# Kernel optimization log

Measured on AMD Instinct MI355X. Metric: run time of the kernel, lower is better.

Reference implementation:

```python
import jax, jax.numpy as jnp
import numpy as np
from jax import lax

BS, L, HID = 16, 512, 768
H, HD, NREG = 12, 64, 8
R2 = 2 * NREG


def setup_inputs() -> dict:
    key = jax.random.key(0)
    ks = jax.random.split(key, 7)
    s = 1.0 / np.sqrt(HID)
    return {
        "hidden_states": jax.random.normal(ks[0], (BS, L, HID), jnp.float32),
        "K1_w": jax.random.normal(ks[1], (H * HD, HID), jnp.float32) * s,
        "K1_b": jnp.zeros((H * HD,), jnp.float32),
        "V1_w": jax.random.normal(ks[2], (H * HD, HID), jnp.float32) * s,
        "V1_b": jnp.zeros((H * HD,), jnp.float32),
        "reading_head": jax.random.normal(ks[3], (H, HD), jnp.float32) * (1.0 / np.sqrt(HD)),
        "bidirection_weight": jnp.ones((1, 1, H, 1, R2), jnp.float32) * (1.0 / R2),
    }


def _softmax_dim1(x):
    # torch: softmax over length dim (1) plus 1/exp(max) residual term
    m = jnp.max(x, axis=1, keepdims=True)
    e = jnp.exp(x - m)
    return e / jnp.sum(e, axis=1, keepdims=True) + jnp.exp(-m)


def _cummax_idx(e):
    # torch.cummax indices over axis=1 for a bool tensor (ties -> latest index):
    # last True index so far; if no True yet, current index.
    ar = jnp.arange(e.shape[1], dtype=jnp.int32)[None, :, None]
    lt = lax.cummax(jnp.where(e, ar, jnp.int32(-1)), axis=1)
    return jnp.where(lt >= 0, lt, ar)


def reference(hidden_states, K1_w, K1_b, V1_w, V1_b, reading_head, bidirection_weight):
    bs, length, _ = hidden_states.shape
    K1 = jax.nn.relu(hidden_states @ K1_w.T + K1_b).reshape(bs, length, H, HD)
    V1 = jax.nn.relu(hidden_states @ V1_w.T + V1_b).reshape(bs, length, H, HD)

    scores = jnp.einsum("blhn,hn->blh", K1, reading_head)
    events = _softmax_dim1(scores) > (1.5 / length)  # (bs, L, H) bool; fwd==bwd for IC1

    col0 = _cummax_idx(events)  # (bs, L, H)
    rolled = jnp.roll(events, -1, axis=1)
    col1 = jnp.flip(512 - _cummax_idx(jnp.flip(rolled, axis=1)), axis=1)
    col1 = col1.at[:, 0].set(0)

    # sequential shift-register scan over length
    e_seq = jnp.moveaxis(events, 1, 0)  # (L, bs, H)
    f_seq = jnp.moveaxis(col0, 1, 0)
    b_seq = jnp.moveaxis(col1, 1, 0)
    row0 = jnp.concatenate(
        [f_seq[0][:, None], b_seq[0][:, None], jnp.zeros((bs, R2, H), jnp.int32)], axis=1
    )  # (bs, R2+2, H)

    def step(row, inp):
        e, f, b = inp
        reg = jnp.where(e[:, None, :], row[:, :-2], row[:, 2:])  # shift-in on event
        new_row = jnp.concatenate([f[:, None], b[:, None], reg], axis=1)
        return new_row, reg

    _, regs = lax.scan(step, row0, (e_seq[1:], f_seq[1:], b_seq[1:]))
    regs = jnp.concatenate([jnp.zeros((1, bs, R2, H), jnp.int32), regs], axis=0)  # (L,bs,R2,H)
    idx = jnp.moveaxis(regs, 0, 1).reshape(bs, length * R2, H)
    idx = jnp.clip(idx, 0, length - 1)

    V2 = jnp.take_along_axis(V1, idx[..., None], axis=1).reshape(bs, length, R2, H, HD)
    w = bidirection_weight.reshape(H, R2)
    return jnp.einsum("blrhd,hr->blhd", V2, w)  # (bs, L, H, HD)
```

## Files before the change

kernel.cpp:

```cpp
#include <hip/hip_runtime.h>
#include <cstdint>
#include <cstddef>

#define BSZ 16
#define LQ  512
#define HIDDIM 768
#define NH  12
#define HD  64
#define R2V 16
#define NTOT 1536
#define MTOT 8192

typedef __bf16 bf16x8 __attribute__((ext_vector_type(8)));
typedef float  f32x4  __attribute__((ext_vector_type(4)));

__device__ inline unsigned short f2bf(float x) {
    union { float f; unsigned u; } c; c.f = x;
    unsigned r = c.u + 0x7fffu + ((c.u >> 16) & 1u);
    return (unsigned short)(r >> 16);
}
__device__ inline float bfl(unsigned u) { return __uint_as_float(u << 16); }
__device__ inline float bfh(unsigned u) { return __uint_as_float(u & 0xffff0000u); }

#define NHS4 1572864
#define NW1  147456
#define NW4  294912

__global__ __launch_bounds__(256) void cast_pack(
    const float* __restrict__ hs,
    const float* __restrict__ Kw, const float* __restrict__ Vw,
    const float* __restrict__ Kb, const float* __restrict__ Vb,
    unsigned short* __restrict__ hsb, unsigned short* __restrict__ Wb,
    float* __restrict__ biasp)
{
    const int i = blockIdx.x * 256 + threadIdx.x;
    float4 v; unsigned short* dst;
    if (i < NHS4) {
        v = ((const float4*)hs)[i];
        dst = hsb + (size_t)i * 4;
    } else {
        const int j = i - NHS4;
        v = (j < NW1) ? ((const float4*)Kw)[j] : ((const float4*)Vw)[j - NW1];
        dst = Wb + (size_t)j * 4;
    }
    ushort4 o;
    o.x = f2bf(v.x); o.y = f2bf(v.y); o.z = f2bf(v.z); o.w = f2bf(v.w);
    *(ushort4*)dst = o;
    if (i < 768) { biasp[i] = Kb[i]; biasp[768 + i] = Vb[i]; }
}

#define TBM 128
#define TBN 128
#define TBK 32
#define KITERS (HIDDIM / TBK)

#define GLD16(g, l) __builtin_amdgcn_global_load_lds( \
    (const __attribute__((address_space(1))) void*)(g), \
    (__attribute__((address_space(3))) void*)(l), 16, 0, 0)

__global__ __launch_bounds__(256) void gemm_mfma(
    const unsigned short* __restrict__ Abf,
    const unsigned short* __restrict__ Wbf,
    const float* __restrict__ biasp,
    unsigned short* __restrict__ K1b, unsigned short* __restrict__ V1b)
{
    __shared__ unsigned short As[2][TBM * TBK];
    __shared__ unsigned short Bs[2][TBN * TBK];

    const int n0   = blockIdx.x * TBN;
    const int m0   = blockIdx.y * TBM;
    const int tid  = threadIdx.x;
    const int wid  = tid >> 6;
    const int lane = tid & 63;
    const int wm   = (wid & 1) * 64;
    const int wn   = (wid >> 1) * 64;

    f32x4 acc[4][4] = {};

    const int r0 = wid * 32;
    const int rA = r0 + (lane >> 2);
    const int kp = (lane & 3) * 8;

    const unsigned short* Ap0 = Abf + (size_t)(m0 + rA) * HIDDIM + kp;
    const unsigned short* Ap1 = Abf + (size_t)(m0 + rA + 16) * HIDDIM + kp;
    const unsigned short* Bp0 = Wbf + (size_t)(n0 + rA) * HIDDIM + kp;
    const unsigned short* Bp1 = Wbf + (size_t)(n0 + rA + 16) * HIDDIM + kp;

    const int fm = lane & 15;
    const int fk = (lane >> 4) * 8;

#define STAGE(buf, kof)                                        \
    do {                                                       \
        GLD16(Ap0 + (kof), &As[buf][r0 * TBK]);                \
        GLD16(Ap1 + (kof), &As[buf][(r0 + 16) * TBK]);         \
        GLD16(Bp0 + (kof), &Bs[buf][r0 * TBK]);                \
        GLD16(Bp1 + (kof), &Bs[buf][(r0 + 16) * TBK]);         \
    } while (0)

    STAGE(0, 0);

    for (int it = 0; it < KITERS; ++it) {
        __syncthreads();
        if (it + 1 < KITERS) STAGE((it + 1) & 1, (it + 1) * TBK);
        const int cb = it & 1;

        bf16x8 af[4], bfr[4];
        #pragma unroll
        for (int mi = 0; mi < 4; ++mi)
            af[mi] = *reinterpret_cast<const bf16x8*>(&As[cb][(wm + mi * 16 + fm) * TBK + fk]);
        #pragma unroll
        for (int ni = 0; ni < 4; ++ni)
            bfr[ni] = *reinterpret_cast<const bf16x8*>(&Bs[cb][(wn + ni * 16 + fm) * TBK + fk]);
        #pragma unroll
        for (int mi = 0; mi < 4; ++mi)
            #pragma unroll
            for (int ni = 0; ni < 4; ++ni)
                acc[mi][ni] = __builtin_amdgcn_mfma_f32_16x16x32_bf16(
                    bfr[ni], af[mi], acc[mi][ni], 0, 0, 0);
    }
#undef STAGE

    const bool isK = (n0 < HIDDIM);
    unsigned short* __restrict__ dst = isK ? K1b : V1b;
    const int nsub = isK ? 0 : HIDDIM;
    const int mloc = lane & 15;
    const int nq   = (lane >> 4) * 4;

    #pragma unroll
    for (int mi = 0; mi < 4; ++mi) {
        const int mg = m0 + wm + mi * 16 + mloc;
        #pragma unroll
        for (int ni = 0; ni < 4; ++ni) {
            const int ng = n0 + wn + ni * 16 + nq;
            float4 bv = *(const float4*)(biasp + ng);
            f32x4 a = acc[mi][ni];
            ushort4 o;
            o.x = f2bf(fmaxf(a[0] + bv.x, 0.f));
            o.y = f2bf(fmaxf(a[1] + bv.y, 0.f));
            o.z = f2bf(fmaxf(a[2] + bv.z, 0.f));
            o.w = f2bf(fmaxf(a[3] + bv.w, 0.f));
            *(ushort4*)(dst + (size_t)mg * HIDDIM + (ng - nsub)) = o;
        }
    }
}

#define SINF (1 << 30)
#define IXP 17

__global__ __launch_bounds__(512) void scan_gather(
    const unsigned short* __restrict__ K1b,
    const unsigned short* __restrict__ V1b,
    const float* __restrict__ rh,
    const float* __restrict__ bw,
    float* __restrict__ out)
{
    const int bh   = blockIdx.x;
    const int b    = bh / NH;
    const int h    = bh % NH;
    const int l    = threadIdx.x;
    const int lane = l & 63;
    const int wid  = l >> 6;

    __shared__ float wredA[8];
    __shared__ float wredB[8];
    __shared__ int   wp0[8];
    __shared__ int   wp1[8];
    __shared__ int   wp2[8];
    __shared__ int   ev[LQ];
    __shared__ int   col0[LQ];
    __shared__ int   col1[LQ];
    __shared__ int   E[LQ];
    __shared__ int   idxs[LQ * IXP];
    __shared__ float wsm[R2V];

    if (l < R2V) wsm[l] = bw[h * R2V + l];

    const unsigned short* krow = K1b + ((size_t)(b * LQ + l)) * HIDDIM + h * HD;
    const float* rrow = rh + h * HD;
    float s = 0.f;
    #pragma unroll
    for (int c8 = 0; c8 < 8; ++c8) {
        uint4 kv = *(const uint4*)(krow + c8 * 8);
        float4 ra = *(const float4*)(rrow + c8 * 8);
        float4 rb = *(const float4*)(rrow + c8 * 8 + 4);
        s += bfl(kv.x) * ra.x + bfh(kv.x) * ra.y
           + bfl(kv.y) * ra.z + bfh(kv.y) * ra.w
           + bfl(kv.z) * rb.x + bfh(kv.z) * rb.y
           + bfl(kv.w) * rb.z + bfh(kv.w) * rb.w;
    }

    float mx = s;
    #pragma unroll
    for (int off = 32; off > 0; off >>= 1) mx = fmaxf(mx, __shfl_xor(mx, off));
    if (lane == 0) wredA[wid] = mx;
    __syncthreads();
    float m = wredA[0];
    #pragma unroll
    for (int i = 1; i < 8; ++i) m = fmaxf(m, wredA[i]);

    const float e = expf(s - m);
    float sm = e;
    #pragma unroll
    for (int off = 32; off > 0; off >>= 1) sm += __shfl_xor(sm, off);
    if (lane == 0) wredB[wid] = sm;
    __syncthreads();
    float ssum = 0.f;
    #pragma unroll
    for (int i = 0; i < 8; ++i) ssum += wredB[i];

    const float p = e / ssum + expf(-m);
    const int event = (p > (1.5f / 512.0f)) ? 1 : 0;
    ev[l] = event;

    int v = event ? l : -1;
    #pragma unroll
    for (int off = 1; off < 64; off <<= 1) {
        int u = __shfl_up(v, off);
        if (lane >= off) v = (u > v) ? u : v;
    }
    if (lane == 63) wp0[wid] = v;
    __syncthreads();
    int pfx = -1;
    for (int i = 0; i < wid; ++i) pfx = (wp0[i] > pfx) ? wp0[i] : pfx;
    v = (pfx > v) ? pfx : v;
    col0[l] = (v >= 0) ? v : l;

    int v1 = ev[(l + 1) & (LQ - 1)] ? l : SINF;
    #pragma unroll
    for (int off = 1; off < 64; off <<= 1) {
        int u = __shfl_down(v1, off);
        if (lane < 64 - off) v1 = (u < v1) ? u : v1;
    }
    if (lane == 0) wp1[wid] = v1;
    __syncthreads();
    int sfx = SINF;
    for (int i = wid + 1; i < 8; ++i) sfx = (wp1[i] < sfx) ? wp1[i] : sfx;
    v1 = (sfx < v1) ? sfx : v1;
    col1[l] = (l == 0) ? 0 : (((v1 < SINF) ? v1 : l) + 1);

    int c = (l >= 1) ? event : 0;
    #pragma unroll
    for (int off = 1; off < 64; off <<= 1) {
        int u = __shfl_up(c, off);
        if (lane >= off) c += u;
    }
    if (lane == 63) wp2[wid] = c;
    __syncthreads();
    for (int i = 0; i < wid; ++i) c += wp2[i];

    if (l >= 1 && event) E[c - 1] = l;
    __syncthreads();

    int* op = &idxs[l * IXP];
    #pragma unroll
    for (int j = 0; j < 8; ++j) {
        const int k = c - 1 - j;
        int f = 0, bb = 0;
        if (k >= 0) {
            const int t = E[k];
            f  = col0[t - 1];
            bb = col1[t - 1];
        }
        op[2 * j]     = min(max(f, 0), LQ - 1);
        op[2 * j + 1] = min(max(bb, 0), LQ - 1);
    }
    __syncthreads();

    const int dsl = lane & 7;
    const size_t vbase = (size_t)b * LQ * HIDDIM + h * HD + dsl * 8;

    for (int round = 0; round < 8; ++round) {
        const int lg = round * 64 + wid * 8 + (lane >> 3);
        const int* ip = &idxs[lg * IXP];
        float a0 = 0.f, a1 = 0.f, a2 = 0.f, a3 = 0.f;
        float a4 = 0.f, a5 = 0.f, a6 = 0.f, a7 = 0.f;
        #pragma unroll 1
        for (int rc = 0; rc < R2V; rc += 4) {
            const int i0 = ip[rc], i1 = ip[rc + 1], i2 = ip[rc + 2], i3 = ip[rc + 3];
            uint4 v0 = *(const uint4*)(V1b + vbase + (size_t)i0 * HIDDIM);
            uint4 vA = *(const uint4*)(V1b + vbase + (size_t)i1 * HIDDIM);
            uint4 vB = *(const uint4*)(V1b + vbase + (size_t)i2 * HIDDIM);
            uint4 vC = *(const uint4*)(V1b + vbase + (size_t)i3 * HIDDIM);
            const float w0 = wsm[rc], w1 = wsm[rc + 1], w2 = wsm[rc + 2], w3 = wsm[rc + 3];
            a0 += w0 * bfl(v0.x); a1 += w0 * bfh(v0.x);
            a2 += w0 * bfl(v0.y); a3 += w0 * bfh(v0.y);
            a4 += w0 * bfl(v0.z); a5 += w0 * bfh(v0.z);
            a6 += w0 * bfl(v0.w); a7 += w0 * bfh(v0.w);
            a0 += w1 * bfl(vA.x); a1 += w1 * bfh(vA.x);
            a2 += w1 * bfl(vA.y); a3 += w1 * bfh(vA.y);
            a4 += w1 * bfl(vA.z); a5 += w1 * bfh(vA.z);
            a6 += w1 * bfl(vA.w); a7 += w1 * bfh(vA.w);
            a0 += w2 * bfl(vB.x); a1 += w2 * bfh(vB.x);
            a2 += w2 * bfl(vB.y); a3 += w2 * bfh(vB.y);
            a4 += w2 * bfl(vB.z); a5 += w2 * bfh(vB.z);
            a6 += w2 * bfl(vB.w); a7 += w2 * bfh(vB.w);
            a0 += w3 * bfl(vC.x); a1 += w3 * bfh(vC.x);
            a2 += w3 * bfl(vC.y); a3 += w3 * bfh(vC.y);
            a4 += w3 * bfl(vC.z); a5 += w3 * bfh(vC.z);
            a6 += w3 * bfl(vC.w); a7 += w3 * bfh(vC.w);
        }
        float* po = out + ((size_t)(b * LQ + lg) * NH + h) * HD + dsl * 8;
        *(float4*)po       = make_float4(a0, a1, a2, a3);
        *((float4*)po + 1) = make_float4(a4, a5, a6, a7);
    }
}

extern "C" void kernel_launch(void* const* d_in, const int* in_sizes, int n_in,
                              void* d_out, int out_size, void* d_ws, size_t ws_size,
                              hipStream_t stream)
{
    (void)in_sizes; (void)n_in; (void)out_size; (void)ws_size;

    const float* hs = (const float*)d_in[0];
    const float* Kw = (const float*)d_in[1];
    const float* Kb = (const float*)d_in[2];
    const float* Vw = (const float*)d_in[3];
    const float* Vb = (const float*)d_in[4];
    const float* rh = (const float*)d_in[5];
    const float* bw = (const float*)d_in[6];
    float* out = (float*)d_out;

    char* ws = (char*)d_ws;
    unsigned short* K1b   = (unsigned short*)(ws);
    unsigned short* V1b   = (unsigned short*)(ws + 12582912);
    unsigned short* hsb   = (unsigned short*)(ws + 25165824);
    unsigned short* Wb    = (unsigned short*)(ws + 37748736);
    float*          biasp = (float*)(ws + 40108032);

    cast_pack<<<(NHS4 + NW4) / 256, 256, 0, stream>>>(hs, Kw, Vw, Kb, Vb, hsb, Wb, biasp);

    dim3 g1(NTOT / TBN, MTOT / TBM);
    gemm_mfma<<<g1, 256, 0, stream>>>(hsb, Wb, biasp, K1b, V1b);

    scan_gather<<<BSZ * NH, LQ, 0, stream>>>(K1b, V1b, rh, bw, out);
}
```

Baseline: 145.7 us.

## Fuse fp32-to-bf16 cast into GEMM tile loads, drop separate cast kernel

Removes the standalone cast_pack kernel. The GEMM now reads fp32 activations and weights directly into registers, converts them to bf16 with packed conversions, and writes them into the double-buffered LDS tiles. Global loads for the next tile are issued before the MFMA work so they overlap with compute. This saves one kernel launch and the write and re-read of bf16 copies in exchiange for reading fp32 (twice the bytes per tile) from global memory on every GEMM block. It also gives up the asynchronous global_load_lds path and adds register pressure under the new occupancy hint of 3.

```diff
diff --git a/kernel.cpp b/kernel.cpp
--- a/kernel.cpp
+++ b/kernel.cpp
@@ -22,31 +22,15 @@
 __device__ inline float bfl(unsigned u) { return __uint_as_float(u << 16); }
 __device__ inline float bfh(unsigned u) { return __uint_as_float(u & 0xffff0000u); }
 
-#define NHS4 1572864
-#define NW1  147456
-#define NW4  294912
-
-__global__ __launch_bounds__(256) void cast_pack(
-    const float* __restrict__ hs,
-    const float* __restrict__ Kw, const float* __restrict__ Vw,
-    const float* __restrict__ Kb, const float* __restrict__ Vb,
-    unsigned short* __restrict__ hsb, unsigned short* __restrict__ Wb,
-    float* __restrict__ biasp)
-{
-    const int i = blockIdx.x * 256 + threadIdx.x;
-    float4 v; unsigned short* dst;
-    if (i < NHS4) {
-        v = ((const float4*)hs)[i];
-        dst = hsb + (size_t)i * 4;
-    } else {
-        const int j = i - NHS4;
-        v = (j < NW1) ? ((const float4*)Kw)[j] : ((const float4*)Vw)[j - NW1];
-        dst = Wb + (size_t)j * 4;
-    }
-    ushort4 o;
-    o.x = f2bf(v.x); o.y = f2bf(v.y); o.z = f2bf(v.z); o.w = f2bf(v.w);
-    *(ushort4*)dst = o;
-    if (i < 768) { biasp[i] = Kb[i]; biasp[768 + i] = Vb[i]; }
+__device__ inline unsigned pk2bf(float x, float y) {
+#if __has_builtin(__builtin_amdgcn_cvt_pk_bf16_f32)
+    typedef __bf16 bf16x2 __attribute__((ext_vector_type(2)));
+    union { bf16x2 v; unsigned u; } c;
+    c.v = __builtin_amdgcn_cvt_pk_bf16_f32(x, y);
+    return c.u;
+#else
+    return (unsigned)f2bf(x) | ((unsigned)f2bf(y) << 16);
+#endif
 }
 
 #define TBM 128
@@ -54,14 +38,10 @@
 #define TBK 32
 #define KITERS (HIDDIM / TBK)
 
-#define GLD16(g, l) __builtin_amdgcn_global_load_lds( \
-    (const __attribute__((address_space(1))) void*)(g), \
-    (__attribute__((address_space(3))) void*)(l), 16, 0, 0)
-
-__global__ __launch_bounds__(256) void gemm_mfma(
-    const unsigned short* __restrict__ Abf,
-    const unsigned short* __restrict__ Wbf,
-    const float* __restrict__ biasp,
+__global__ __launch_bounds__(256, 3) void gemm_fused(
+    const float* __restrict__ hs,
+    const float* __restrict__ Kw, const float* __restrict__ Vw,
+    const float* __restrict__ Kb, const float* __restrict__ Vb,
     unsigned short* __restrict__ K1b, unsigned short* __restrict__ V1b)
 {
     __shared__ unsigned short As[2][TBM * TBK];
@@ -75,34 +55,65 @@
     const int wm   = (wid & 1) * 64;
     const int wn   = (wid >> 1) * 64;
 
+    const bool isK = (n0 < HIDDIM);
+    const float* __restrict__ Wsrc = isK ? Kw : Vw;
+    const float* __restrict__ bias = isK ? Kb : Vb;
+    const int ncol0 = isK ? n0 : (n0 - HIDDIM);
+
     f32x4 acc[4][4] = {};
 
     const int r0 = wid * 32;
-    const int rA = r0 + (lane >> 2);
-    const int kp = (lane & 3) * 8;
-
-    const unsigned short* Ap0 = Abf + (size_t)(m0 + rA) * HIDDIM + kp;
-    const unsigned short* Ap1 = Abf + (size_t)(m0 + rA + 16) * HIDDIM + kp;
-    const unsigned short* Bp0 = Wbf + (size_t)(n0 + rA) * HIDDIM + kp;
-    const unsigned short* Bp1 = Wbf + (size_t)(n0 + rA + 16) * HIDDIM + kp;
+    const int rA = r0 + (lane >> 1);
+    const int kh = (lane & 1) * 16;
+
+    const float* Aptr = hs   + (size_t)(m0 + rA) * HIDDIM + kh;
+    const float* Bptr = Wsrc + (size_t)(ncol0 + rA) * HIDDIM + kh;
+
+    uint4* AsD = (uint4*)&As[0][rA * TBK + kh];
+    uint4* BsD = (uint4*)&Bs[0][rA * TBK + kh];
+    const int bufStride16 = (TBM * TBK) / 8;
+
+    float4 ar0, ar1, ar2, ar3, br0, br1, br2, br3;
+
+#define LOADREGS(kof)                                     \
+    do {                                                  \
+        ar0 = *(const float4*)(Aptr + (kof));             \
+        ar1 = *(const float4*)(Aptr + (kof) + 4);         \
+        ar2 = *(const float4*)(Aptr + (kof) + 8);         \
+        ar3 = *(const float4*)(Aptr + (kof) + 12);        \
+        br0 = *(const float4*)(Bptr + (kof));             \
+        br1 = *(const float4*)(Bptr + (kof) + 4);         \
+        br2 = *(const float4*)(Bptr + (kof) + 8);         \
+        br3 = *(const float4*)(Bptr + (kof) + 12);        \
+    } while (0)
+
+#define CVTSTORE(buf)                                                         \
+    do {                                                                      \
+        uint4 p;                                                              \
+        p.x = pk2bf(ar0.x, ar0.y); p.y = pk2bf(ar0.z, ar0.w);                 \
+        p.z = pk2bf(ar1.x, ar1.y); p.w = pk2bf(ar1.z, ar1.w);                 \
+        AsD[(buf) * bufStride16] = p;                                         \
+        p.x = pk2bf(ar2.x, ar2.y); p.y = pk2bf(ar2.z, ar2.w);                 \
+        p.z = pk2bf(ar3.x, ar3.y); p.w = pk2bf(ar3.z, ar3.w);                 \
+        AsD[(buf) * bufStride16 + 1] = p;                                     \
+        p.x = pk2bf(br0.x, br0.y); p.y = pk2bf(br0.z, br0.w);                 \
+        p.z = pk2bf(br1.x, br1.y); p.w = pk2bf(br1.z, br1.w);                 \
+        BsD[(buf) * bufStride16] = p;                                         \
+        p.x = pk2bf(br2.x, br2.y); p.y = pk2bf(br2.z, br2.w);                 \
+        p.z = pk2bf(br3.x, br3.y); p.w = pk2bf(br3.z, br3.w);                 \
+        BsD[(buf) * bufStride16 + 1] = p;                                     \
+    } while (0)
 
     const int fm = lane & 15;
     const int fk = (lane >> 4) * 8;
 
-#define STAGE(buf, kof)                                        \
-    do {                                                       \
-        GLD16(Ap0 + (kof), &As[buf][r0 * TBK]);                \
-        GLD16(Ap1 + (kof), &As[buf][(r0 + 16) * TBK]);         \
-        GLD16(Bp0 + (kof), &Bs[buf][r0 * TBK]);                \
-        GLD16(Bp1 + (kof), &Bs[buf][(r0 + 16) * TBK]);         \
-    } while (0)
-
-    STAGE(0, 0);
+    LOADREGS(0);
+    CVTSTORE(0);
 
     for (int it = 0; it < KITERS; ++it) {
         __syncthreads();
-        if (it + 1 < KITERS) STAGE((it + 1) & 1, (it + 1) * TBK);
         const int cb = it & 1;
+        if (it + 1 < KITERS) LOADREGS((it + 1) * TBK);
 
         bf16x8 af[4], bfr[4];
         #pragma unroll
@@ -117,12 +128,13 @@
             for (int ni = 0; ni < 4; ++ni)
                 acc[mi][ni] = __builtin_amdgcn_mfma_f32_16x16x32_bf16(
                     bfr[ni], af[mi], acc[mi][ni], 0, 0, 0);
-    }
-#undef STAGE
-
-    const bool isK = (n0 < HIDDIM);
+
+        if (it + 1 < KITERS) CVTSTORE(cb ^ 1);
+    }
+#undef LOADREGS
+#undef CVTSTORE
+
     unsigned short* __restrict__ dst = isK ? K1b : V1b;
-    const int nsub = isK ? 0 : HIDDIM;
     const int mloc = lane & 15;
     const int nq   = (lane >> 4) * 4;
 
@@ -131,15 +143,15 @@
         const int mg = m0 + wm + mi * 16 + mloc;
         #pragma unroll
         for (int ni = 0; ni < 4; ++ni) {
-            const int ng = n0 + wn + ni * 16 + nq;
-            float4 bv = *(const float4*)(biasp + ng);
+            const int col = ncol0 + wn + ni * 16 + nq;
+            float4 bv = *(const float4*)(bias + col);
             f32x4 a = acc[mi][ni];
             ushort4 o;
             o.x = f2bf(fmaxf(a[0] + bv.x, 0.f));
             o.y = f2bf(fmaxf(a[1] + bv.y, 0.f));
             o.z = f2bf(fmaxf(a[2] + bv.z, 0.f));
             o.w = f2bf(fmaxf(a[3] + bv.w, 0.f));
-            *(ushort4*)(dst + (size_t)mg * HIDDIM + (ng - nsub)) = o;
+            *(ushort4*)(dst + (size_t)mg * HIDDIM + col) = o;
         }
     }
 }
@@ -321,16 +333,11 @@
     float* out = (float*)d_out;
 
     char* ws = (char*)d_ws;
-    unsigned short* K1b   = (unsigned short*)(ws);
-    unsigned short* V1b   = (unsigned short*)(ws + 12582912);
-    unsigned short* hsb   = (unsigned short*)(ws + 25165824);
-    unsigned short* Wb    = (unsigned short*)(ws + 37748736);
-    float*          biasp = (float*)(ws + 40108032);
-
-    cast_pack<<<(NHS4 + NW4) / 256, 256, 0, stream>>>(hs, Kw, Vw, Kb, Vb, hsb, Wb, biasp);
+    unsigned short* K1b = (unsigned short*)(ws);
+    unsigned short* V1b = (unsigned short*)(ws + 12582912);
 
     dim3 g1(NTOT / TBN, MTOT / TBM);
-    gemm_mfma<<<g1, 256, 0, stream>>>(hsb, Wb, biasp, K1b, V1b);
+    gemm_fused<<<g1, 256, 0, stream>>>(hs, Kw, Vw, Kb, Vb, K1b, V1b);
 
     scan_gather<<<BSZ * NH, LQ, 0, stream>>>(K1b, V1b, rh, bw, out);
 }
```

New measurement: 161.4 us. 10.8% more time.

## Store V1 in fp32 and halve GEMM N-tile to 64

Applied to the files above, without the earlier changes.

The GEMM tile width drops from 128 to 64 columns, which doubles the block count and cuts the accumulators per wave. The V projection is now written as fp32 instead of bf16, and the gather reads fp32 directly, which removes the bf16 unpacking. The cost is twice the V1 write traffic and twice the gather read bytes. Weaker per-block data reuse in the GEMM also adds LDS/global traffic.

```diff
diff --git a/kernel.cpp b/kernel.cpp
--- a/kernel.cpp
+++ b/kernel.cpp
@@ -50,7 +50,7 @@
 }
 
 #define TBM 128
-#define TBN 128
+#define TBN 64
 #define TBK 32
 #define KITERS (HIDDIM / TBK)
 
@@ -62,7 +62,8 @@
     const unsigned short* __restrict__ Abf,
     const unsigned short* __restrict__ Wbf,
     const float* __restrict__ biasp,
-    unsigned short* __restrict__ K1b, unsigned short* __restrict__ V1b)
+    unsigned short* __restrict__ K1b,
+    float* __restrict__ V1f)
 {
     __shared__ unsigned short As[2][TBM * TBK];
     __shared__ unsigned short Bs[2][TBN * TBK];
@@ -73,73 +74,88 @@
     const int wid  = tid >> 6;
     const int lane = tid & 63;
     const int wm   = (wid & 1) * 64;
-    const int wn   = (wid >> 1) * 64;
-
-    f32x4 acc[4][4] = {};
-
-    const int r0 = wid * 32;
-    const int rA = r0 + (lane >> 2);
+    const int wn   = (wid >> 1) * 32;
+
+    f32x4 acc[4][2] = {};
+
+    const int rA = wid * 32 + (lane >> 2);
     const int kp = (lane & 3) * 8;
-
     const unsigned short* Ap0 = Abf + (size_t)(m0 + rA) * HIDDIM + kp;
     const unsigned short* Ap1 = Abf + (size_t)(m0 + rA + 16) * HIDDIM + kp;
-    const unsigned short* Bp0 = Wbf + (size_t)(n0 + rA) * HIDDIM + kp;
-    const unsigned short* Bp1 = Wbf + (size_t)(n0 + rA + 16) * HIDDIM + kp;
+    const int rB = wid * 16 + (lane >> 2);
+    const unsigned short* Bp0 = Wbf + (size_t)(n0 + rB) * HIDDIM + kp;
+
+#define STAGE(buf, kof)                                            \
+    do {                                                           \
+        GLD16(Ap0 + (kof), &As[buf][(wid * 32) * TBK]);            \
+        GLD16(Ap1 + (kof), &As[buf][(wid * 32 + 16) * TBK]);       \
+        GLD16(Bp0 + (kof), &Bs[buf][(wid * 16) * TBK]);            \
+    } while (0)
 
     const int fm = lane & 15;
     const int fk = (lane >> 4) * 8;
 
-#define STAGE(buf, kof)                                        \
-    do {                                                       \
-        GLD16(Ap0 + (kof), &As[buf][r0 * TBK]);                \
-        GLD16(Ap1 + (kof), &As[buf][(r0 + 16) * TBK]);         \
-        GLD16(Bp0 + (kof), &Bs[buf][r0 * TBK]);                \
-        GLD16(Bp1 + (kof), &Bs[buf][(r0 + 16) * TBK]);         \
-    } while (0)
-
     STAGE(0, 0);
 
     for (int it = 0; it < KITERS; ++it) {
         __syncthreads();
-        if (it + 1 < KITERS) STAGE((it + 1) & 1, (it + 1) * TBK);
         const int cb = it & 1;
-
-        bf16x8 af[4], bfr[4];
+        if (it + 1 < KITERS) STAGE(cb ^ 1, (it + 1) * TBK);
+
+        bf16x8 af[4], bfr[2];
         #pragma unroll
         for (int mi = 0; mi < 4; ++mi)
             af[mi] = *reinterpret_cast<const bf16x8*>(&As[cb][(wm + mi * 16 + fm) * TBK + fk]);
         #pragma unroll
-        for (int ni = 0; ni < 4; ++ni)
+        for (int ni = 0; ni < 2; ++ni)
             bfr[ni] = *reinterpret_cast<const bf16x8*>(&Bs[cb][(wn + ni * 16 + fm) * TBK + fk]);
         #pragma unroll
         for (int mi = 0; mi < 4; ++mi)
             #pragma unroll
-            for (int ni = 0; ni < 4; ++ni)
+            for (int ni = 0; ni < 2; ++ni)
                 acc[mi][ni] = __builtin_amdgcn_mfma_f32_16x16x32_bf16(
                     bfr[ni], af[mi], acc[mi][ni], 0, 0, 0);
     }
 #undef STAGE
 
     const bool isK = (n0 < HIDDIM);
-    unsigned short* __restrict__ dst = isK ? K1b : V1b;
-    const int nsub = isK ? 0 : HIDDIM;
+    const int ncol0 = isK ? n0 : (n0 - HIDDIM);
     const int mloc = lane & 15;
     const int nq   = (lane >> 4) * 4;
 
-    #pragma unroll
-    for (int mi = 0; mi < 4; ++mi) {
-        const int mg = m0 + wm + mi * 16 + mloc;
-        #pragma unroll
-        for (int ni = 0; ni < 4; ++ni) {
-            const int ng = n0 + wn + ni * 16 + nq;
-            float4 bv = *(const float4*)(biasp + ng);
-            f32x4 a = acc[mi][ni];
-            ushort4 o;
-            o.x = f2bf(fmaxf(a[0] + bv.x, 0.f));
-            o.y = f2bf(fmaxf(a[1] + bv.y, 0.f));
-            o.z = f2bf(fmaxf(a[2] + bv.z, 0.f));
-            o.w = f2bf(fmaxf(a[3] + bv.w, 0.f));
-            *(ushort4*)(dst + (size_t)mg * HIDDIM + (ng - nsub)) = o;
+    if (isK) {
+        #pragma unroll
+        for (int mi = 0; mi < 4; ++mi) {
+            const int mg = m0 + wm + mi * 16 + mloc;
+            #pragma unroll
+            for (int ni = 0; ni < 2; ++ni) {
+                const int col = ncol0 + wn + ni * 16 + nq;
+                float4 bv = *(const float4*)(biasp + (isK ? 0 : HIDDIM) + col);
+                f32x4 a = acc[mi][ni];
+                ushort4 o;
+                o.x = f2bf(fmaxf(a[0] + bv.x, 0.f));
+                o.y = f2bf(fmaxf(a[1] + bv.y, 0.f));
+                o.z = f2bf(fmaxf(a[2] + bv.z, 0.f));
+                o.w = f2bf(fmaxf(a[3] + bv.w, 0.f));
+                *(ushort4*)(K1b + (size_t)mg * HIDDIM + col) = o;
+            }
+        }
+    } else {
+        #pragma unroll
+        for (int mi = 0; mi < 4; ++mi) {
+            const int mg = m0 + wm + mi * 16 + mloc;
+            #pragma unroll
+            for (int ni = 0; ni < 2; ++ni) {
+                const int col = ncol0 + wn + ni * 16 + nq;
+                float4 bv = *(const float4*)(biasp + HIDDIM + col);
+                f32x4 a = acc[mi][ni];
+                float4 o;
+                o.x = fmaxf(a[0] + bv.x, 0.f);
+                o.y = fmaxf(a[1] + bv.y, 0.f);
+                o.z = fmaxf(a[2] + bv.z, 0.f);
+                o.w = fmaxf(a[3] + bv.w, 0.f);
+                *(float4*)(V1f + (size_t)mg * HIDDIM + col) = o;
+            }
         }
     }
 }
@@ -149,7 +165,7 @@
 
 __global__ __launch_bounds__(512) void scan_gather(
     const unsigned short* __restrict__ K1b,
-    const unsigned short* __restrict__ V1b,
+    const float* __restrict__ V1f,
     const float* __restrict__ rh,
     const float* __restrict__ bw,
     float* __restrict__ out)
@@ -272,36 +288,32 @@
     for (int round = 0; round < 8; ++round) {
         const int lg = round * 64 + wid * 8 + (lane >> 3);
         const int* ip = &idxs[lg * IXP];
-        float a0 = 0.f, a1 = 0.f, a2 = 0.f, a3 = 0.f;
-        float a4 = 0.f, a5 = 0.f, a6 = 0.f, a7 = 0.f;
+        float4 accA = make_float4(0.f, 0.f, 0.f, 0.f);
+        float4 accB = make_float4(0.f, 0.f, 0.f, 0.f);
         #pragma unroll 1
         for (int rc = 0; rc < R2V; rc += 4) {
             const int i0 = ip[rc], i1 = ip[rc + 1], i2 = ip[rc + 2], i3 = ip[rc + 3];
-            uint4 v0 = *(const uint4*)(V1b + vbase + (size_t)i0 * HIDDIM);
-            uint4 vA = *(const uint4*)(V1b + vbase + (size_t)i1 * HIDDIM);
-            uint4 vB = *(const uint4*)(V1b + vbase + (size_t)i2 * HIDDIM);
-            uint4 vC = *(const uint4*)(V1b + vbase + (size_t)i3 * HIDDIM);
             const float w0 = wsm[rc], w1 = wsm[rc + 1], w2 = wsm[rc + 2], w3 = wsm[rc + 3];
-            a0 += w0 * bfl(v0.x); a1 += w0 * bfh(v0.x);
-            a2 += w0 * bfl(v0.y); a3 += w0 * bfh(v0.y);
-            a4 += w0 * bfl(v0.z); a5 += w0 * bfh(v0.z);
-            a6 += w0 * bfl(v0.w); a7 += w0 * bfh(v0.w);
-            a0 += w1 * bfl(vA.x); a1 += w1 * bfh(vA.x);
-            a2 += w1 * bfl(vA.y); a3 += w1 * bfh(vA.y);
-            a4 += w1 * bfl(vA.z); a5 += w1 * bfh(vA.z);
-            a6 += w1 * bfl(vA.w); a7 += w1 * bfh(vA.w);
-            a0 += w2 * bfl(vB.x); a1 += w2 * bfh(vB.x);
-            a2 += w2 * bfl(vB.y); a3 += w2 * bfh(vB.y);
-            a4 += w2 * bfl(vB.z); a5 += w2 * bfh(vB.z);
-            a6 += w2 * bfl(vB.w); a7 += w2 * bfh(vB.w);
-            a0 += w3 * bfl(vC.x); a1 += w3 * bfh(vC.x);
-            a2 += w3 * bfl(vC.y); a3 += w3 * bfh(vC.y);
-            a4 += w3 * bfl(vC.z); a5 += w3 * bfh(vC.z);
-            a6 += w3 * bfl(vC.w); a7 += w3 * bfh(vC.w);
+            const float* p0 = V1f + vbase + (size_t)i0 * HIDDIM;
+            const float* p1 = V1f + vbase + (size_t)i1 * HIDDIM;
+            const float* p2 = V1f + vbase + (size_t)i2 * HIDDIM;
+            const float* p3 = V1f + vbase + (size_t)i3 * HIDDIM;
+            float4 a0 = *(const float4*)p0, b0 = *(const float4*)(p0 + 4);
+            float4 a1 = *(const float4*)p1, b1 = *(const float4*)(p1 + 4);
+            float4 a2 = *(const float4*)p2, b2 = *(const float4*)(p2 + 4);
+            float4 a3 = *(const float4*)p3, b3 = *(const float4*)(p3 + 4);
+            accA.x += w0 * a0.x + w1 * a1.x + w2 * a2.x + w3 * a3.x;
+            accA.y += w0 * a0.y + w1 * a1.y + w2 * a2.y + w3 * a3.y;
+            accA.z += w0 * a0.z + w1 * a1.z + w2 * a2.z + w3 * a3.z;
+            accA.w += w0 * a0.w + w1 * a1.w + w2 * a2.w + w3 * a3.w;
+            accB.x += w0 * b0.x + w1 * b1.x + w2 * b2.x + w3 * b3.x;
+            accB.y += w0 * b0.y + w1 * b1.y + w2 * b2.y + w3 * b3.y;
+            accB.z += w0 * b0.z + w1 * b1.z + w2 * b2.z + w3 * b3.z;
+            accB.w += w0 * b0.w + w1 * b1.w + w2 * b2.w + w3 * b3.w;
         }
         float* po = out + ((size_t)(b * LQ + lg) * NH + h) * HD + dsl * 8;
-        *(float4*)po       = make_float4(a0, a1, a2, a3);
-        *((float4*)po + 1) = make_float4(a4, a5, a6, a7);
+        *(float4*)po       = accA;
+        *((float4*)po + 1) = accB;
     }
 }
 
@@ -322,15 +334,15 @@
 
     char* ws = (char*)d_ws;
     unsigned short* K1b   = (unsigned short*)(ws);
-    unsigned short* V1b   = (unsigned short*)(ws + 12582912);
-    unsigned short* hsb   = (unsigned short*)(ws + 25165824);
-    unsigned short* Wb    = (unsigned short*)(ws + 37748736);
-    float*          biasp = (float*)(ws + 40108032);
+    float*          V1f   = (float*)(ws + 12582912);
+    unsigned short* hsb   = (unsigned short*)(ws + 37748736);
+    unsigned short* Wb    = (unsigned short*)(ws + 50331648);
+    float*          biasp = (float*)(ws + 52690944);
 
     cast_pack<<<(NHS4 + NW4) / 256, 256, 0, stream>>>(hs, Kw, Vw, Kb, Vb, hsb, Wb, biasp);
 
     dim3 g1(NTOT / TBN, MTOT / TBM);
-    gemm_mfma<<<g1, 256, 0, stream>>>(hsb, Wb, biasp, K1b, V1b);
-
-    scan_gather<<<BSZ * NH, LQ, 0, stream>>>(K1b, V1b, rh, bw, out);
-}
+    gemm_mfma<<<g1, 256, 0, stream>>>(hsb, Wb, biasp, K1b, V1f);
+
+    scan_gather<<<BSZ * NH, LQ, 0, stream>>>(K1b, V1f, rh, bw, out);
+}
```

Result: slower. 156.4 us (+7.3%).
